# Kernel tuning notes

Measured on AMD Instinct MI355X. Metric: run time of the kernel, lower is better.

The kernel has to match this reference:

```python
import jax, jax.numpy as jnp
import numpy as np

B, M, N, D = 1, 128, 256, 256   # batch, msa rows, residues, node dim
DE = 128                        # edge (pair) dim
H, DH = 8, 64                   # heads, dim_head
INNER = H * DH


def setup_inputs() -> dict:
    key = jax.random.key(0)
    ks = jax.random.split(key, 10)
    s = 0.02
    return {
        "x": jax.random.normal(ks[0], (B, M, N, D), jnp.float32),
        "edges": jax.random.normal(ks[1], (B, N, N, DE), jnp.float32),
        "mask": jnp.ones((B, M, N), dtype=bool),
        "ln_g": jnp.ones((D,), jnp.float32),
        "ln_b": jnp.zeros((D,), jnp.float32),
        "Wq": jax.random.normal(ks[2], (D, INNER), jnp.float32) * s,
        "Wkv": jax.random.normal(ks[3], (D, 2 * INNER), jnp.float32) * s,
        "Wg": jax.random.normal(ks[4], (D, INNER), jnp.float32) * s,
        "bg": jnp.ones((INNER,), jnp.float32),
        "Wo": jax.random.normal(ks[5], (INNER, D), jnp.float32) * s,
        "bo": jnp.zeros((D,), jnp.float32),
        "Wb": jax.random.normal(ks[6], (DE, H), jnp.float32) * s,
    }


def reference(x, edges, mask, ln_g, ln_b, Wq, Wkv, Wg, bg, Wo, bo, Wb):
    b, m, n, d = x.shape
    scale = DH ** -0.5
    # LayerNorm over node dim (biased variance, eps=1e-5 as torch default)
    mu = x.mean(-1, keepdims=True)
    var = x.var(-1, keepdims=True)
    xn = (x - mu) / jnp.sqrt(var + 1e-5) * ln_g + ln_b

    # pair bias: [b, h, i, j], shared across MSA rows
    bias = jnp.einsum('bijc,ch->bhij', edges, Wb)

    # projections, split heads: [b, m, n, h, dh]
    q = jnp.einsum('bmnd,de->bmne', xn, Wq).reshape(b, m, n, H, DH) * scale
    kv = jnp.einsum('bmnd,de->bmne', xn, Wkv)
    k = kv[..., :INNER].reshape(b, m, n, H, DH)
    v = kv[..., INNER:].reshape(b, m, n, H, DH)

    # tied queries: mean over MSA rows (global_query_attn, tie_dim=m)
    qm = q.mean(axis=1)  # [b, n, h, dh]
    dots = jnp.einsum('bihd,bmjhd->bmhij', qm, k) + bias[:, None]  # [b,m,h,i,j]

    pair_mask = mask[:, :, None, :, None] & mask[:, :, None, None, :]
    neg = -jnp.finfo(dots.dtype).max
    dots = jnp.where(pair_mask, dots, neg)
    attn = jax.nn.softmax(dots, axis=-1)

    out = jnp.einsum('bmhij,bmjhd->bmihd', attn, v).reshape(b, m, n, INNER)
    gates = jax.nn.sigmoid(jnp.einsum('bmnd,de->bmne', xn, Wg) + bg)
    out = out * gates
    return jnp.einsum('bmne,ed->bmnd', out, Wo) + bo
```

## Files before the change

### kernel.cpp

```cpp
#include <hip/hip_runtime.h>
#include <stdint.h>


#define DEV __device__ __forceinline__

typedef __attribute__((ext_vector_type(8))) short bf16x8;
typedef __attribute__((ext_vector_type(4))) float f32x4;

DEV short f2bf(float f) {
  union { float f; uint32_t u; } v; v.f = f;
  uint32_t r = v.u + 0x7fffu + ((v.u >> 16) & 1u);
  return (short)(r >> 16);
}
DEV float bf2f(short s) {
  union { uint32_t u; float f; } v; v.u = ((uint32_t)(uint16_t)s) << 16;
  return v.f;
}

#define GLDS16(gp, lp) __builtin_amdgcn_global_load_lds( \
    (__attribute__((address_space(1))) void*)(gp),       \
    (__attribute__((address_space(3))) void*)(lp), 16, 0, 0)

__global__ __launch_bounds__(256) void k_ln(const float* __restrict__ x,
                                            const float* __restrict__ g,
                                            const float* __restrict__ b,
                                            short* __restrict__ xn) {
  int wave = threadIdx.x >> 6, lane = threadIdx.x & 63;
  long row = (long)blockIdx.x * 4 + wave;
  const float* xr = x + row * 256;
  float4 v = ((const float4*)xr)[lane];
  float s = v.x + v.y + v.z + v.w;
  float sq = v.x*v.x + v.y*v.y + v.z*v.z + v.w*v.w;
#pragma unroll
  for (int o = 1; o < 64; o <<= 1) { s += __shfl_xor(s, o); sq += __shfl_xor(sq, o); }
  float mu = s * (1.f/256.f);
  float var = sq * (1.f/256.f) - mu*mu;
  float rstd = rsqrtf(var + 1e-5f);
  float4 gg = ((const float4*)g)[lane];
  float4 bb = ((const float4*)b)[lane];
  short4 o4;
  o4.x = f2bf((v.x-mu)*rstd*gg.x + bb.x);
  o4.y = f2bf((v.y-mu)*rstd*gg.y + bb.y);
  o4.z = f2bf((v.z-mu)*rstd*gg.z + bb.z);
  o4.w = f2bf((v.w-mu)*rstd*gg.w + bb.w);
  ((short4*)(xn + row * 256))[lane] = o4;
}

__global__ __launch_bounds__(256) void k_wt(const float* __restrict__ Wq,
                                            const float* __restrict__ Wkv,
                                            const float* __restrict__ Wg,
                                            const float* __restrict__ Wo,
                                            short* __restrict__ WT,
                                            short* __restrict__ WoT) {
  int idx = blockIdx.x * 256 + threadIdx.x;
  if (idx < 2048 * 256) {
    int n = idx >> 8, k = idx & 255;
    float v;
    if (n < 512)       v = Wq[k * 512 + n];
    else if (n < 1536) v = Wkv[k * 1024 + (n - 512)];
    else               v = Wg[k * 512 + (n - 1536)];
    WT[idx] = f2bf(v);
  } else {
    int j = idx - 2048 * 256;
    int k = j & 511;
    WoT[j] = f2bf(Wo[k * 256 + (j >> 9)]);
  }
}

__global__ __launch_bounds__(256) void k_bias(const float* __restrict__ edges,
                                              const float* __restrict__ Wb,
                                              float* __restrict__ biasF) {
  int pair = blockIdx.x * 4 + (threadIdx.x >> 6);
  int lane = threadIdx.x & 63;
  const float* e = edges + (long)pair * 128;
  float a0 = e[lane], a1 = e[lane + 64];
  float acc[8];
#pragma unroll
  for (int h = 0; h < 8; ++h)
    acc[h] = a0 * Wb[lane * 8 + h] + a1 * Wb[(lane + 64) * 8 + h];
#pragma unroll
  for (int o = 1; o < 64; o <<= 1) {
#pragma unroll
    for (int h = 0; h < 8; ++h) acc[h] += __shfl_xor(acc[h], o);
  }
  if (lane == 0) {
    int i = pair >> 8, j = pair & 255;
    long base = ((long)(i >> 4) * 16 + (j >> 4)) * 256 +
                (((i >> 2) & 3) * 16 + (j & 15)) * 4 + (i & 3);
#pragma unroll
    for (int h = 0; h < 8; ++h) biasF[(long)h * 65536 + base] = acc[h];
  }
}

__global__ __launch_bounds__(256) void k_xbar(const short* __restrict__ xn,
                                              float* __restrict__ xbar) {
  int i = blockIdx.x, d = threadIdx.x;
  const short* p = xn + (long)i * 256 + d;
  float s = 0.f;
#pragma unroll 4
  for (int mm = 0; mm < 128; ++mm) s += bf2f(p[(long)mm * 65536]);
  xbar[i * 256 + d] = s * (1.f / 128.f);
}

__global__ __launch_bounds__(256) void k_qmg(const float* __restrict__ xbar,
                                             const short* __restrict__ WT,
                                             short* __restrict__ qm) {
  int i = blockIdx.x;
  int e0 = threadIdx.x;
  const float* xb = xbar + i * 256;
  float acc0 = 0.f, acc1 = 0.f;
  for (int d = 0; d < 256; d += 8) {
    bf16x8 w0 = *(const bf16x8*)&WT[e0 * 256 + d];
    bf16x8 w1 = *(const bf16x8*)&WT[(e0 + 256) * 256 + d];
#pragma unroll
    for (int t = 0; t < 8; ++t) {
      float xv = xb[d + t];
      acc0 += xv * bf2f(w0[t]);
      acc1 += xv * bf2f(w1[t]);
    }
  }
  qm[((e0 >> 6) * 256 + i) * 64 + (e0 & 63)] = f2bf(acc0 * 0.125f);
  int e1 = e0 + 256;
  qm[((e1 >> 6) * 256 + i) * 64 + (e1 & 63)] = f2bf(acc1 * 0.125f);
}

__global__ __launch_bounds__(256, 3) void k_proj(const short* __restrict__ A,
                                                 const short* __restrict__ B,
                                                 short* __restrict__ kRM,
                                                 short* __restrict__ vT,
                                                 short* __restrict__ gRM,
                                                 const float* __restrict__ bg) {
  __shared__ short As[2][128 * 32];
  __shared__ short Bs[2][128 * 32];
  int tid = threadIdx.x;
  int wave = tid >> 6, lane = tid & 63;
  int quad = lane >> 4, l15 = lane & 15;
  long row0 = (long)blockIdx.y * 128;
  int col0 = 512 + blockIdx.x * 128;
  int wi = (wave >> 1) * 64, wj = (wave & 1) * 64;
  f32x4 acc[4][4] = {};
  const short* Ab = A + row0 * 256;
  const short* Bb = B + (long)col0 * 256;
  int r0 = tid >> 2, gc0 = tid & 3;
  int g0 = (gc0 ^ ((r0 >> 1) & 3)) * 8;
  int g1 = (gc0 ^ (((r0 + 64) >> 1) & 3)) * 8;

#define PSTAGE(buf, k0) do {                                          \
    GLDS16(Ab + (long)r0 * 256 + (k0) + g0,        &As[buf][tid * 8]);          \
    GLDS16(Ab + (long)(r0 + 64) * 256 + (k0) + g1, &As[buf][(tid + 256) * 8]);  \
    GLDS16(Bb + (long)r0 * 256 + (k0) + g0,        &Bs[buf][tid * 8]);          \
    GLDS16(Bb + (long)(r0 + 64) * 256 + (k0) + g1, &Bs[buf][(tid + 256) * 8]);  \
  } while (0)

  PSTAGE(0, 0);
  for (int it = 0; it < 8; ++it) {
    int cur = it & 1;
    __syncthreads();
    if (it < 7) PSTAGE(1 - cur, (it + 1) * 32);
    bf16x8 a[4], b[4];
#pragma unroll
    for (int t = 0; t < 4; ++t) {
      int ra = wi + t * 16 + l15;
      int rb = wj + t * 16 + l15;
      a[t] = *(const bf16x8*)&As[cur][ra * 32 + ((quad ^ ((ra >> 1) & 3)) * 8)];
      b[t] = *(const bf16x8*)&Bs[cur][rb * 32 + ((quad ^ ((rb >> 1) & 3)) * 8)];
    }
#pragma unroll
    for (int ti = 0; ti < 4; ++ti)
#pragma unroll
      for (int tj = 0; tj < 4; ++tj)
        acc[ti][tj] = __builtin_amdgcn_mfma_f32_16x16x32_bf16(a[ti], b[tj], acc[ti][tj], 0, 0, 0);
  }
#undef PSTAGE

  int rg = col0 >> 9;
#pragma unroll
  for (int ti = 0; ti < 4; ++ti)
#pragma unroll
    for (int tj = 0; tj < 4; ++tj) {
      int gcol = col0 + wj + tj * 16 + l15;
      long grow = row0 + wi + ti * 16 + quad * 4;
      if (rg == 3) {
#pragma unroll
        for (int r = 0; r < 4; ++r) {
          float v = 1.f / (1.f + __expf(-(acc[ti][tj][r] + bg[gcol - 1536])));
          gRM[(grow + r) * 512 + (gcol - 1536)] = f2bf(v);
        }
      } else if (rg == 1) {
#pragma unroll
        for (int r = 0; r < 4; ++r)
          kRM[(grow + r) * 512 + (gcol - 512)] = f2bf(acc[ti][tj][r]);
      } else {
        short4 pk;
        pk.x = f2bf(acc[ti][tj][0]); pk.y = f2bf(acc[ti][tj][1]);
        pk.z = f2bf(acc[ti][tj][2]); pk.w = f2bf(acc[ti][tj][3]);
        *(short4*)&vT[(long)(gcol - 1024) * 32768 + grow] = pk;
      }
    }
}

__global__ __launch_bounds__(512, 4) void k_attn(const short* __restrict__ qm,
                                                 const short* __restrict__ kRM,
                                                 const short* __restrict__ vT,
                                                 const short* __restrict__ gRM,
                                                 const float* __restrict__ biasF,
                                                 short* __restrict__ outA) {
  __shared__ short kL[256 * 64];
  __shared__ short vL[64 * 256];
  __shared__ short pL[8 * 16 * 64];
  int m = blockIdx.x, h = blockIdx.y;
  int tid = threadIdx.x;
  int wave = tid >> 6, lane = tid & 63;
  int quad = lane >> 4, l15 = lane & 15;
  int l7 = l15 & 7;

  const short* kg_ = kRM + ((long)m * 256) * 512 + h * 64;
  const short* vg_ = vT + (long)(h * 64) * 32768 + m * 256;
#pragma unroll
  for (int it = 0; it < 4; ++it) {
    int slot = it * 512 + tid;
    int row = slot >> 3;
    int g = (slot & 7) ^ (row & 7);
    GLDS16(kg_ + (long)row * 512 + g * 8, &kL[slot * 8]);
    int d = slot >> 5;
    int jg = (slot & 31) ^ (d & 7);
    GLDS16(vg_ + (long)d * 32768 + jg * 8, &vL[slot * 8]);
  }

  const short* qmh = qm + h * (256 * 64);
  bf16x8 aq[2][2];
#pragma unroll
  for (int ti = 0; ti < 2; ++ti)
#pragma unroll
    for (int ks = 0; ks < 2; ++ks)
      aq[ti][ks] = *(const bf16x8*)&qmh[(wave * 32 + ti * 16 + l15) * 64 + ks * 32 + quad * 8];

  f32x4 o[2][4] = {};
  float lrow[2][4] = {};
  const float* bF = biasF + ((long)h * 16 + wave * 2) * 16 * 256 + lane * 4;

  __syncthreads();

  for (int jc = 0; jc < 4; ++jc) {
    f32x4 s[2][4];
#pragma unroll
    for (int ti = 0; ti < 2; ++ti)
#pragma unroll
      for (int tj = 0; tj < 4; ++tj)
        s[ti][tj] = *(const f32x4*)&bF[((long)ti * 16 + jc * 4 + tj) * 256];
#pragma unroll
    for (int tj = 0; tj < 4; ++tj) {
      int jrow = jc * 64 + tj * 16 + l15;
      bf16x8 b0 = *(const bf16x8*)&kL[jrow * 64 + ((quad ^ l7) * 8)];
      bf16x8 b1 = *(const bf16x8*)&kL[jrow * 64 + (((4 + quad) ^ l7) * 8)];
#pragma unroll
      for (int ti = 0; ti < 2; ++ti) {
        s[ti][tj] = __builtin_amdgcn_mfma_f32_16x16x32_bf16(aq[ti][0], b0, s[ti][tj], 0, 0, 0);
        s[ti][tj] = __builtin_amdgcn_mfma_f32_16x16x32_bf16(aq[ti][1], b1, s[ti][tj], 0, 0, 0);
      }
    }

#pragma unroll
    for (int ti = 0; ti < 2; ++ti) {
#pragma unroll
      for (int r = 0; r < 4; ++r) {
        int rloc = quad * 4 + r;
#pragma unroll
        for (int tj = 0; tj < 4; ++tj) {
          float p = __expf(s[ti][tj][r]);
          lrow[ti][r] += p;
          int col = tj * 16 + l15;
          int slot = (col >> 3) ^ (rloc & 7);
          pL[wave * 1024 + rloc * 64 + slot * 8 + (col & 7)] = f2bf(p);
        }
      }
      bf16x8 ap0 = *(const bf16x8*)&pL[wave * 1024 + l15 * 64 + ((quad ^ l7) * 8)];
      bf16x8 ap1 = *(const bf16x8*)&pL[wave * 1024 + l15 * 64 + (((4 + quad) ^ l7) * 8)];
#pragma unroll
      for (int td = 0; td < 4; ++td) {
        int drow = td * 16 + l15;
        bf16x8 bv0 = *(const bf16x8*)&vL[drow * 256 + (jc * 8 + (quad ^ l7)) * 8];
        bf16x8 bv1 = *(const bf16x8*)&vL[drow * 256 + (jc * 8 + ((4 + quad) ^ l7)) * 8];
        o[ti][td] = __builtin_amdgcn_mfma_f32_16x16x32_bf16(ap0, bv0, o[ti][td], 0, 0, 0);
        o[ti][td] = __builtin_amdgcn_mfma_f32_16x16x32_bf16(ap1, bv1, o[ti][td], 0, 0, 0);
      }
    }
  }

#pragma unroll
  for (int ti = 0; ti < 2; ++ti)
#pragma unroll
    for (int r = 0; r < 4; ++r) {
      float l = lrow[ti][r];
#pragma unroll
      for (int off = 1; off < 16; off <<= 1) l += __shfl_xor(l, off);
      float inv = 1.f / l;
      int i = wave * 32 + ti * 16 + quad * 4 + r;
      long rowoff = (long)m * 256 + i;
#pragma unroll
      for (int td = 0; td < 4; ++td) {
        int dh = td * 16 + l15;
        float gv = bf2f(gRM[rowoff * 512 + h * 64 + dh]);
        outA[rowoff * 512 + h * 64 + dh] = f2bf(o[ti][td][r] * inv * gv);
      }
    }
}

__global__ __launch_bounds__(256, 3) void k_out(const short* __restrict__ A,
                                                const short* __restrict__ B,
                                                float* __restrict__ out,
                                                const float* __restrict__ bo) {
  __shared__ short As[2][128 * 32];
  __shared__ short Bs[2][128 * 32];
  int tid = threadIdx.x;
  int wave = tid >> 6, lane = tid & 63;
  int quad = lane >> 4, l15 = lane & 15;
  long row0 = (long)blockIdx.y * 128;
  int col0 = blockIdx.x * 128;
  int wi = (wave >> 1) * 64, wj = (wave & 1) * 64;
  f32x4 acc[4][4] = {};
  const short* Ab = A + row0 * 512;
  const short* Bb = B + (long)col0 * 512;
  int r0 = tid >> 2, gc0 = tid & 3;
  int g0 = (gc0 ^ ((r0 >> 1) & 3)) * 8;
  int g1 = (gc0 ^ (((r0 + 64) >> 1) & 3)) * 8;

#define OSTAGE(buf, k0) do {                                          \
    GLDS16(Ab + (long)r0 * 512 + (k0) + g0,        &As[buf][tid * 8]);          \
    GLDS16(Ab + (long)(r0 + 64) * 512 + (k0) + g1, &As[buf][(tid + 256) * 8]);  \
    GLDS16(Bb + (long)r0 * 512 + (k0) + g0,        &Bs[buf][tid * 8]);          \
    GLDS16(Bb + (long)(r0 + 64) * 512 + (k0) + g1, &Bs[buf][(tid + 256) * 8]);  \
  } while (0)

  OSTAGE(0, 0);
  for (int it = 0; it < 16; ++it) {
    int cur = it & 1;
    __syncthreads();
    if (it < 15) OSTAGE(1 - cur, (it + 1) * 32);
    bf16x8 a[4], b[4];
#pragma unroll
    for (int t = 0; t < 4; ++t) {
      int ra = wi + t * 16 + l15;
      int rb = wj + t * 16 + l15;
      a[t] = *(const bf16x8*)&As[cur][ra * 32 + ((quad ^ ((ra >> 1) & 3)) * 8)];
      b[t] = *(const bf16x8*)&Bs[cur][rb * 32 + ((quad ^ ((rb >> 1) & 3)) * 8)];
    }
#pragma unroll
    for (int ti = 0; ti < 4; ++ti)
#pragma unroll
      for (int tj = 0; tj < 4; ++tj)
        acc[ti][tj] = __builtin_amdgcn_mfma_f32_16x16x32_bf16(a[ti], b[tj], acc[ti][tj], 0, 0, 0);
  }
#undef OSTAGE

#pragma unroll
  for (int ti = 0; ti < 4; ++ti)
#pragma unroll
    for (int tj = 0; tj < 4; ++tj)
#pragma unroll
      for (int r = 0; r < 4; ++r) {
        long grow = row0 + wi + ti * 16 + quad * 4 + r;
        int gcol = col0 + wj + tj * 16 + l15;
        out[grow * 256 + gcol] = acc[ti][tj][r] + bo[gcol];
      }
}

extern "C" void kernel_launch(void* const* d_in, const int* in_sizes, int n_in,
                              void* d_out, int out_size, void* d_ws, size_t ws_size,
                              hipStream_t stream) {
  (void)in_sizes; (void)n_in; (void)out_size; (void)ws_size;
  const float* x     = (const float*)d_in[0];
  const float* edges = (const float*)d_in[1];
  const float* ln_g  = (const float*)d_in[3];
  const float* ln_b  = (const float*)d_in[4];
  const float* Wq    = (const float*)d_in[5];
  const float* Wkv   = (const float*)d_in[6];
  const float* Wg    = (const float*)d_in[7];
  const float* bg    = (const float*)d_in[8];
  const float* Wo    = (const float*)d_in[9];
  const float* bo    = (const float*)d_in[10];
  const float* Wb    = (const float*)d_in[11];
  float* out = (float*)d_out;

  char* ws = (char*)d_ws;
  short* xn    = (short*)ws;  ws += 32768L * 256 * 2;
  short* WT    = (short*)ws;  ws += 2048L * 256 * 2;
  short* WoT   = (short*)ws;  ws += 256L * 512 * 2;
  short* kRM   = (short*)ws;  ws += 32768L * 512 * 2;
  short* vT    = (short*)ws;  ws += 512L * 32768 * 2;
  short* gRM   = (short*)ws;  ws += 32768L * 512 * 2;
  float* biasF = (float*)ws;  ws += 8L * 256 * 256 * 4;
  float* xbar  = (float*)ws;  ws += 256L * 256 * 4;
  short* qmb   = (short*)ws;  ws += 8L * 256 * 64 * 2;
  short* outA  = (short*)ws;  ws += 32768L * 512 * 2;

  k_ln<<<8192, 256, 0, stream>>>(x, ln_g, ln_b, xn);
  k_wt<<<2560, 256, 0, stream>>>(Wq, Wkv, Wg, Wo, WT, WoT);
  k_bias<<<16384, 256, 0, stream>>>(edges, Wb, biasF);
  k_xbar<<<256, 256, 0, stream>>>(xn, xbar);
  k_qmg<<<256, 256, 0, stream>>>(xbar, WT, qmb);
  k_proj<<<dim3(12, 256), 256, 0, stream>>>(xn, WT, kRM, vT, gRM, bg);
  k_attn<<<dim3(128, 8), 512, 0, stream>>>(qmb, kRM, vT, gRM, biasF, outA);
  k_out<<<dim3(2, 256), 256, 0, stream>>>(outA, WoT, out, bo);
}
```

Baseline: 294.0 us.

## Vectorize GEMM epilogue stores, remap proj blocks, widen xbar/qmg parallelism

Several changes: k_xbar splits the 128-row reduction across 4 thread groups with an LDS reduction, and k_qmg uses 512 threads with one output each. k_proj remaps block IDs so that blocks sharing an XCD process nearby tiles, and raises the occupancy hint to 4 blocks per CU. For the k/g projections and the output GEMM, the MFMA operands are swapped so each lane holds 4 consecutive columns, which turns scattered scalar stores into short4/float4 vector stores. The aim is to cut uncoalesced epilogue writes and the low parallelism in the small kernels, at the cost of branching inside k_proj and possible register pressure under the new launch bound.

```diff
diff --git a/kernel.cpp b/kernel.cpp
--- a/kernel.cpp
+++ b/kernel.cpp
@@ -92,39 +92,37 @@
   }
 }
 
-__global__ __launch_bounds__(256) void k_xbar(const short* __restrict__ xn,
-                                              float* __restrict__ xbar) {
-  int i = blockIdx.x, d = threadIdx.x;
-  const short* p = xn + (long)i * 256 + d;
+__global__ __launch_bounds__(1024) void k_xbar(const short* __restrict__ xn,
+                                               float* __restrict__ xbar) {
+  __shared__ float red[3][256];
+  int i = blockIdx.x;
+  int d = threadIdx.x & 255, mc = threadIdx.x >> 8;
+  const short* p = xn + (long)mc * 32 * 65536 + (long)i * 256 + d;
   float s = 0.f;
-#pragma unroll 4
-  for (int mm = 0; mm < 128; ++mm) s += bf2f(p[(long)mm * 65536]);
-  xbar[i * 256 + d] = s * (1.f / 128.f);
-}
-
-__global__ __launch_bounds__(256) void k_qmg(const float* __restrict__ xbar,
+#pragma unroll 8
+  for (int mm = 0; mm < 32; ++mm) s += bf2f(p[(long)mm * 65536]);
+  if (mc) red[mc - 1][d] = s;
+  __syncthreads();
+  if (mc == 0)
+    xbar[i * 256 + d] = (s + red[0][d] + red[1][d] + red[2][d]) * (1.f / 128.f);
+}
+
+__global__ __launch_bounds__(512) void k_qmg(const float* __restrict__ xbar,
                                              const short* __restrict__ WT,
                                              short* __restrict__ qm) {
   int i = blockIdx.x;
-  int e0 = threadIdx.x;
+  int e = threadIdx.x;
   const float* xb = xbar + i * 256;
-  float acc0 = 0.f, acc1 = 0.f;
+  float acc = 0.f;
   for (int d = 0; d < 256; d += 8) {
-    bf16x8 w0 = *(const bf16x8*)&WT[e0 * 256 + d];
-    bf16x8 w1 = *(const bf16x8*)&WT[(e0 + 256) * 256 + d];
-#pragma unroll
-    for (int t = 0; t < 8; ++t) {
-      float xv = xb[d + t];
-      acc0 += xv * bf2f(w0[t]);
-      acc1 += xv * bf2f(w1[t]);
-    }
-  }
-  qm[((e0 >> 6) * 256 + i) * 64 + (e0 & 63)] = f2bf(acc0 * 0.125f);
-  int e1 = e0 + 256;
-  qm[((e1 >> 6) * 256 + i) * 64 + (e1 & 63)] = f2bf(acc1 * 0.125f);
-}
-
-__global__ __launch_bounds__(256, 3) void k_proj(const short* __restrict__ A,
+    bf16x8 w = *(const bf16x8*)&WT[e * 256 + d];
+#pragma unroll
+    for (int t = 0; t < 8; ++t) acc += xb[d + t] * bf2f(w[t]);
+  }
+  qm[((e >> 6) * 256 + i) * 64 + (e & 63)] = f2bf(acc * 0.125f);
+}
+
+__global__ __launch_bounds__(256, 4) void k_proj(const short* __restrict__ A,
                                                  const short* __restrict__ B,
                                                  short* __restrict__ kRM,
                                                  short* __restrict__ vT,
@@ -135,8 +133,13 @@
   int tid = threadIdx.x;
   int wave = tid >> 6, lane = tid & 63;
   int quad = lane >> 4, l15 = lane & 15;
-  long row0 = (long)blockIdx.y * 128;
-  int col0 = 512 + blockIdx.x * 128;
+  int bid = blockIdx.y * 12 + blockIdx.x;
+  int wg  = (bid & 7) * 384 + (bid >> 3);
+  int bx = wg % 12, by = wg / 12;
+  long row0 = (long)by * 128;
+  int col0 = 512 + bx * 128;
+  int rg = col0 >> 9;
+  bool swapped = (rg != 2);
   int wi = (wave >> 1) * 64, wj = (wave & 1) * 64;
   f32x4 acc[4][4] = {};
   const short* Ab = A + row0 * 256;
@@ -165,38 +168,62 @@
       a[t] = *(const bf16x8*)&As[cur][ra * 32 + ((quad ^ ((ra >> 1) & 3)) * 8)];
       b[t] = *(const bf16x8*)&Bs[cur][rb * 32 + ((quad ^ ((rb >> 1) & 3)) * 8)];
     }
+    if (swapped) {
+#pragma unroll
+      for (int ti = 0; ti < 4; ++ti)
+#pragma unroll
+        for (int tj = 0; tj < 4; ++tj)
+          acc[ti][tj] = __builtin_amdgcn_mfma_f32_16x16x32_bf16(b[tj], a[ti], acc[ti][tj], 0, 0, 0);
+    } else {
+#pragma unroll
+      for (int ti = 0; ti < 4; ++ti)
+#pragma unroll
+        for (int tj = 0; tj < 4; ++tj)
+          acc[ti][tj] = __builtin_amdgcn_mfma_f32_16x16x32_bf16(a[ti], b[tj], acc[ti][tj], 0, 0, 0);
+    }
+  }
+#undef PSTAGE
+
+  if (rg == 2) {
 #pragma unroll
     for (int ti = 0; ti < 4; ++ti)
 #pragma unroll
-      for (int tj = 0; tj < 4; ++tj)
-        acc[ti][tj] = __builtin_amdgcn_mfma_f32_16x16x32_bf16(a[ti], b[tj], acc[ti][tj], 0, 0, 0);
-  }
-#undef PSTAGE
-
-  int rg = col0 >> 9;
-#pragma unroll
-  for (int ti = 0; ti < 4; ++ti)
-#pragma unroll
-    for (int tj = 0; tj < 4; ++tj) {
-      int gcol = col0 + wj + tj * 16 + l15;
-      long grow = row0 + wi + ti * 16 + quad * 4;
-      if (rg == 3) {
-#pragma unroll
-        for (int r = 0; r < 4; ++r) {
-          float v = 1.f / (1.f + __expf(-(acc[ti][tj][r] + bg[gcol - 1536])));
-          gRM[(grow + r) * 512 + (gcol - 1536)] = f2bf(v);
-        }
-      } else if (rg == 1) {
-#pragma unroll
-        for (int r = 0; r < 4; ++r)
-          kRM[(grow + r) * 512 + (gcol - 512)] = f2bf(acc[ti][tj][r]);
-      } else {
+      for (int tj = 0; tj < 4; ++tj) {
+        int gcol = col0 + wj + tj * 16 + l15;
+        long grow = row0 + wi + ti * 16 + quad * 4;
         short4 pk;
         pk.x = f2bf(acc[ti][tj][0]); pk.y = f2bf(acc[ti][tj][1]);
         pk.z = f2bf(acc[ti][tj][2]); pk.w = f2bf(acc[ti][tj][3]);
         *(short4*)&vT[(long)(gcol - 1024) * 32768 + grow] = pk;
       }
-    }
+  } else if (rg == 1) {
+#pragma unroll
+    for (int ti = 0; ti < 4; ++ti)
+#pragma unroll
+      for (int tj = 0; tj < 4; ++tj) {
+        long token = row0 + wi + ti * 16 + l15;
+        int gco = col0 + wj + tj * 16 + quad * 4 - 512;
+        short4 pk;
+        pk.x = f2bf(acc[ti][tj][0]); pk.y = f2bf(acc[ti][tj][1]);
+        pk.z = f2bf(acc[ti][tj][2]); pk.w = f2bf(acc[ti][tj][3]);
+        *(short4*)&kRM[token * 512 + gco] = pk;
+      }
+  } else {
+#pragma unroll
+    for (int ti = 0; ti < 4; ++ti)
+#pragma unroll
+      for (int tj = 0; tj < 4; ++tj) {
+        long token = row0 + wi + ti * 16 + l15;
+        int gco = col0 + wj + tj * 16 + quad * 4 - 1536;
+        float4 b4 = *(const float4*)&bg[gco];
+        short4 pk;
+        pk.x = f2bf(1.f / (1.f + __expf(-(acc[ti][tj][0] + b4.x))));
+        pk.y = f2bf(1.f / (1.f + __expf(-(acc[ti][tj][1] + b4.y))));
+        pk.z = f2bf(1.f / (1.f + __expf(-(acc[ti][tj][2] + b4.z))));
+        pk.w = f2bf(1.f / (1.f + __expf(-(acc[ti][tj][3] + b4.w))));
+        *(short4*)&gRM[token * 512 + gco] = pk;
+      }
+  }
 }
 
 __global__ __launch_bounds__(512, 4) void k_attn(const short* __restrict__ qm,
@@ -349,20 +376,24 @@
     for (int ti = 0; ti < 4; ++ti)
 #pragma unroll
       for (int tj = 0; tj < 4; ++tj)
-        acc[ti][tj] = __builtin_amdgcn_mfma_f32_16x16x32_bf16(a[ti], b[tj], acc[ti][tj], 0, 0, 0);
+        acc[ti][tj] = __builtin_amdgcn_mfma_f32_16x16x32_bf16(b[tj], a[ti], acc[ti][tj], 0, 0, 0);
   }
 #undef OSTAGE
 
 #pragma unroll
   for (int ti = 0; ti < 4; ++ti)
 #pragma unroll
-    for (int tj = 0; tj < 4; ++tj)
-#pragma unroll
-      for (int r = 0; r < 4; ++r) {
-        long grow = row0 + wi + ti * 16 + quad * 4 + r;
-        int gcol = col0 + wj + tj * 16 + l15;
-        out[grow * 256 + gcol] = acc[ti][tj][r] + bo[gcol];
-      }
+    for (int tj = 0; tj < 4; ++tj) {
+      long token = row0 + wi + ti * 16 + l15;
+      int gco = col0 + wj + tj * 16 + quad * 4;
+      float4 b4 = *(const float4*)&bo[gco];
+      float4 r4;
+      r4.x = acc[ti][tj][0] + b4.x;
+      r4.y = acc[ti][tj][1] + b4.y;
+      r4.z = acc[ti][tj][2] + b4.z;
+      r4.w = acc[ti][tj][3] + b4.w;
+      *(float4*)&out[token * 256 + gco] = r4;
+    }
 }
 
 extern "C" void kernel_launch(void* const* d_in, const int* in_sizes, int n_in,
@@ -397,8 +428,8 @@
   k_ln<<<8192, 256, 0, stream>>>(x, ln_g, ln_b, xn);
   k_wt<<<2560, 256, 0, stream>>>(Wq, Wkv, Wg, Wo, WT, WoT);
   k_bias<<<16384, 256, 0, stream>>>(edges, Wb, biasF);
-  k_xbar<<<256, 256, 0, stream>>>(xn, xbar);
-  k_qmg<<<256, 256, 0, stream>>>(xbar, WT, qmb);
+  k_xbar<<<256, 1024, 0, stream>>>(xn, xbar);
+  k_qmg<<<256, 512, 0, stream>>>(xbar, WT, qmb);
   k_proj<<<dim3(12, 256), 256, 0, stream>>>(xn, WT, kRM, vT, gRM, bg);
   k_attn<<<dim3(128, 8), 512, 0, stream>>>(qmb, kRM, vT, gRM, biasF, outA);
   k_out<<<dim3(2, 256), 256, 0, stream>>>(outA, WoT, out, bo);
```

Result: slower. 482.1 us (+64.0%).
